# Optimization experiments

Measured on AMD Instinct MI355X. Metric: run time of the kernel, lower is better.

The kernel has to match this reference:

```python
import jax, jax.numpy as jnp
import numpy as np

H = 1024          # hidden_size
M = 512           # moe_intermediate_size
E = 16            # n_routed_experts
TOP_K = 4         # num_experts_per_tok
N_GROUP = 4
TOPK_GROUP = 2
SCALE = 2.5       # routed_scaling_factor
B, S = 2, 1024


def setup_inputs() -> dict:
    key = jax.random.key(0)
    ks = jax.random.split(key, 9)
    sc_h = 1.0 / np.sqrt(H)
    sc_m = 1.0 / np.sqrt(M)
    return {
        "hidden_states": jax.random.normal(ks[0], (B, S, H), jnp.float32),
        "gate_kernel": jax.random.normal(ks[1], (H, E), jnp.float32) * sc_h,
        "gate_bias": jax.random.normal(ks[2], (E,), jnp.float32) * 0.01,
        "w_gate": jax.random.normal(ks[3], (E, H, M), jnp.float32) * sc_h,
        "w_up": jax.random.normal(ks[4], (E, H, M), jnp.float32) * sc_h,
        "w_down": jax.random.normal(ks[5], (E, M, H), jnp.float32) * sc_m,
        "sw_gate": jax.random.normal(ks[6], (H, 2 * M), jnp.float32) * sc_h,
        "sw_up": jax.random.normal(ks[7], (H, 2 * M), jnp.float32) * sc_h,
        "sw_down": jax.random.normal(ks[8], (2 * M, H), jnp.float32) * (1.0 / np.sqrt(2 * M)),
    }


def _gate(x2d, gate_kernel, gate_bias):
    # x2d: [N, H]
    n = x2d.shape[0]
    logits = jnp.dot(x2d.astype(jnp.float32), gate_kernel.astype(jnp.float32))  # [N, E]
    scores = jax.nn.sigmoid(logits)
    scores_for_choice = scores + gate_bias  # noaux_tc correction bias
    # group-limited top-k: sum of top-2 scores per group
    group_scores = scores_for_choice.reshape(n, N_GROUP, E // N_GROUP)
    top2 = jax.lax.top_k(group_scores, k=2)[0]
    group_sum = jnp.sum(top2, axis=-1)                       # [N, G]
    group_idx = jax.lax.top_k(group_sum, k=TOPK_GROUP)[1]    # [N, topk_group]
    group_mask = jnp.zeros_like(group_sum).at[jnp.arange(n)[:, None], group_idx].set(1.0)
    score_mask = jnp.repeat(group_mask[:, :, None], E // N_GROUP, axis=2).reshape(n, E)
    masked_scores = jnp.where(score_mask > 0, scores_for_choice, 0.0)
    topk_weight, topk_idx = jax.lax.top_k(masked_scores, k=TOP_K)
    # norm_topk_prob
    topk_weight = topk_weight / (jnp.sum(topk_weight, axis=-1, keepdims=True) + 1e-20)
    topk_weight = topk_weight * SCALE
    return topk_idx, topk_weight


def reference(hidden_states, gate_kernel, gate_bias, w_gate, w_up, w_down,
              sw_gate, sw_up, sw_down):
    orig_shape = hidden_states.shape
    x = hidden_states.reshape(-1, orig_shape[-1])  # [N, H]
    topk_idx, topk_weight = _gate(x, gate_kernel, gate_bias)
    # combine weight per (token, expert): sum_k (topk_idx==e) * topk_weight
    onehot = (topk_idx[:, :, None] == jnp.arange(E)[None, None, :]).astype(topk_weight.dtype)
    combine = jnp.einsum('nke,nk->ne', onehot, topk_weight)  # [N, E]
    # dense per-expert MLP (faithful to moe_infer which runs every expert)
    g = jnp.einsum('nh,ehm->enm', x, w_gate)   # [E, N, M]
    u = jnp.einsum('nh,ehm->enm', x, w_up)
    inter = jax.nn.silu(g) * u
    y_e = jnp.einsum('enm,emh->enh', inter, w_down)          # [E, N, H]
    y = jnp.einsum('ne,enh->nh', combine, y_e)               # [N, H]
    # shared-expert path
    shared = jnp.dot(jax.nn.silu(jnp.dot(x, sw_gate)) * jnp.dot(x, sw_up), sw_down)
    return (y + shared).reshape(orig_shape)
```

## Files before the change

kernel.cpp:

```cpp
#include <hip/hip_runtime.h>
#include <hip/hip_bf16.h>
#include <cstdint>

#define HID    1024
#define MID    512
#define NEXP   16
#define NTOKS  2048
#define TOPKE  4
#define RSCALE 2.5f
#define CSTR   16

typedef __attribute__((ext_vector_type(8))) short  bf16x8;
typedef __attribute__((ext_vector_type(8))) ushort u16x8;
typedef __attribute__((ext_vector_type(4))) float  f32x4;

__device__ __forceinline__ ushort f2bf(float f){
  unsigned u = __float_as_uint(f);
  u += 0x7fffu + ((u >> 16) & 1u);
  return (ushort)(u >> 16);
}
__device__ __forceinline__ float bf2f(ushort h){ return __uint_as_float(((unsigned)h) << 16); }

#define GLD16(g, l) __builtin_amdgcn_global_load_lds( \
    (const __attribute__((address_space(1))) unsigned int*)(g), \
    (__attribute__((address_space(3))) unsigned int*)(l), 16, 0, 0)

__global__ __launch_bounds__(256) void k_route(const float* __restrict__ x,
                                               const float* __restrict__ gk,
                                               const float* __restrict__ gb,
                                               int* __restrict__ counts,
                                               int* __restrict__ tidx,
                                               float* __restrict__ tw)
{
  __shared__ float sc[16][16];
  __shared__ int lcnt[NEXP];
  const int tid = threadIdx.x;
  const int tl  = tid >> 4;
  const int e   = tid & 15;
  const int t   = blockIdx.x * 16 + tl;

  float acc = 0.f;
  const float* xr = x + (size_t)t * HID;
  for (int h = 0; h < HID; h += 4){
    f32x4 xv = *reinterpret_cast<const f32x4*>(xr + h);
    acc += xv[0] * gk[(h+0)*NEXP + e];
    acc += xv[1] * gk[(h+1)*NEXP + e];
    acc += xv[2] * gk[(h+2)*NEXP + e];
    acc += xv[3] * gk[(h+3)*NEXP + e];
  }
  sc[tl][e] = 1.f / (1.f + expf(-acc)) + gb[e];
  if (tid < NEXP) lcnt[tid] = 0;
  __syncthreads();

  if (tid < 16){
    const int tt = blockIdx.x * 16 + tid;
    float s4[NEXP];
    #pragma unroll
    for (int i = 0; i < NEXP; ++i) s4[i] = sc[tid][i];
    float gs[4];
    #pragma unroll
    for (int g = 0; g < 4; ++g){
      float m1 = -1e30f, m2 = -1e30f;
      #pragma unroll
      for (int j = 0; j < 4; ++j){
        float v = s4[g*4+j];
        if (v > m1){ m2 = m1; m1 = v; } else if (v > m2){ m2 = v; }
      }
      gs[g] = m1 + m2;
    }
    int g1 = 0;
    for (int g = 1; g < 4; ++g) if (gs[g] > gs[g1]) g1 = g;
    int g2 = -1;
    for (int g = 0; g < 4; ++g){
      if (g == g1) continue;
      if (g2 < 0 || gs[g] > gs[g2]) g2 = g;
    }
    float ms[NEXP];
    #pragma unroll
    for (int i = 0; i < NEXP; ++i){
      int g = i >> 2;
      ms[i] = (g == g1 || g == g2) ? s4[i] : 0.0f;
    }
    bool used[NEXP];
    #pragma unroll
    for (int i = 0; i < NEXP; ++i) used[i] = false;
    int sel[TOPKE]; float val[TOPKE]; float denom = 0.f;
    #pragma unroll
    for (int k = 0; k < TOPKE; ++k){
      int be = -1; float bv = -1e30f;
      for (int i = 0; i < NEXP; ++i){
        if (used[i]) continue;
        if (ms[i] > bv){ bv = ms[i]; be = i; }
      }
      used[be] = true; sel[k] = be; val[k] = bv; denom += bv;
    }
    float inv = RSCALE / (denom + 1e-20f);
    #pragma unroll
    for (int k = 0; k < TOPKE; ++k){
      tidx[tt*TOPKE + k] = sel[k];
      tw  [tt*TOPKE + k] = val[k] * inv;
      atomicAdd(&lcnt[sel[k]], 1);
    }
  }
  __syncthreads();
  if (tid < NEXP && lcnt[tid]) atomicAdd(&counts[tid * CSTR], lcnt[tid]);
}

__global__ void k_scan(const int* __restrict__ counts, int* __restrict__ offs,
                       int* __restrict__ cursor)
{
  if (threadIdx.x == 0){
    int s = 0;
    for (int e = 0; e < NEXP; ++e){ offs[e] = s; s += counts[e * CSTR]; }
    offs[NEXP] = s;
  }
  if (threadIdx.x < NEXP) cursor[threadIdx.x * CSTR] = 0;
}

__global__ __launch_bounds__(256) void k_place(const int* __restrict__ tidx,
                                               const float* __restrict__ tw,
                                               const int* __restrict__ offs,
                                               int* __restrict__ cursor,
                                               int* __restrict__ tlist,
                                               float* __restrict__ wlist,
                                               int* __restrict__ pos)
{
  __shared__ int lcnt[NEXP];
  __shared__ int lbase[NEXP];
  const int tid = threadIdx.x;
  const int t = blockIdx.x * 256 + tid;
  if (tid < NEXP) lcnt[tid] = 0;
  __syncthreads();
  int sel[TOPKE]; float w4[TOPKE]; int ls[TOPKE];
  #pragma unroll
  for (int k = 0; k < TOPKE; ++k){
    sel[k] = tidx[t*TOPKE + k];
    w4[k]  = tw[t*TOPKE + k];
    ls[k]  = atomicAdd(&lcnt[sel[k]], 1);
  }
  __syncthreads();
  if (tid < NEXP) lbase[tid] = atomicAdd(&cursor[tid * CSTR], lcnt[tid]);
  __syncthreads();
  #pragma unroll
  for (int k = 0; k < TOPKE; ++k){
    int p = offs[sel[k]] + lbase[sel[k]] + ls[k];
    tlist[p] = t;
    wlist[p] = w4[k];
    pos[t*TOPKE + k] = p;
  }
}

__global__ __launch_bounds__(256) void k_cvt(const float* __restrict__ in,
                                             ushort* __restrict__ out, int n8)
{
  int i = blockIdx.x * 256 + threadIdx.x;
  if (i >= n8) return;
  f32x4 a = *reinterpret_cast<const f32x4*>(in + (size_t)i*8);
  f32x4 b = *reinterpret_cast<const f32x4*>(in + (size_t)i*8 + 4);
  u16x8 o;
  o[0]=f2bf(a[0]); o[1]=f2bf(a[1]); o[2]=f2bf(a[2]); o[3]=f2bf(a[3]);
  o[4]=f2bf(b[0]); o[5]=f2bf(b[1]); o[6]=f2bf(b[2]); o[7]=f2bf(b[3]);
  *reinterpret_cast<u16x8*>(out + (size_t)i*8) = o;
}

__global__ __launch_bounds__(256) void k_tr(const float* __restrict__ in,
                                            ushort* __restrict__ out, int K, int N)
{
  const int e = blockIdx.z;
  in  += (size_t)e * K * N;
  out += (size_t)e * K * N;
  const int kb = blockIdx.y * 64, nb = blockIdx.x * 64;
  __shared__ ushort T[64 * 68];
  const int t = threadIdx.x;
  const int r = t >> 4, c4 = (t & 15) * 4;
  #pragma unroll
  for (int i = 0; i < 4; ++i){
    f32x4 v = *reinterpret_cast<const f32x4*>(in + (size_t)(kb + r + i*16) * N + nb + c4);
    #pragma unroll
    for (int j = 0; j < 4; ++j)
      T[(c4 + j) * 68 + r + i*16] = f2bf(v[j]);
  }
  __syncthreads();
  #pragma unroll
  for (int i = 0; i < 4; ++i){
    int n = r + i*16;
    ushort4 o = *reinterpret_cast<const ushort4*>(&T[n * 68 + c4]);
    *reinterpret_cast<ushort4*>(out + (size_t)(nb + n) * K + kb + c4) = o;
  }
}

__global__ __launch_bounds__(512) void k_mm0(
    const ushort* __restrict__ xb,
    ushort* __restrict__ i_s, ushort* __restrict__ i_r,
    const ushort* __restrict__ swgT, const ushort* __restrict__ swuT,
    const ushort* __restrict__ wgT,  const ushort* __restrict__ wuT,
    const int* __restrict__ counts, const int* __restrict__ offs,
    const int* __restrict__ tlist)
{
  const int z = blockIdx.z;
  const bool routed = (z > 0);
  const int e = z - 1;
  const int N = routed ? 512 : 1024;
  const int nbase = blockIdx.x * 128;
  if (nbase >= N) return;
  const int mbase = blockIdx.y * 128;
  int cnt = NTOKS, aoff = 0;
  if (routed){
    cnt = counts[e * CSTR];
    if (mbase >= cnt) return;
    aoff = offs[e];
  }
  const ushort* Bg = routed ? (wgT + (size_t)e * MID * HID) : swgT;
  const ushort* Bu = routed ? (wuT + (size_t)e * MID * HID) : swuT;
  ushort* O = routed ? i_r : i_s;

  __shared__ __align__(16) ushort Sh[3 * 128 * 64];

  const int tid = threadIdx.x;
  const int l   = tid & 63;
  const int w   = tid >> 6;
  const int wm  = w >> 2;
  const int wn  = w & 3;

  const int rl     = l >> 3;
  const int srcOff = 8 * ((l & 7) ^ rl);

  const ushort* srcP[6];
  #pragma unroll
  for (int j = 0; j < 6; ++j){
    int g = w * 6 + j;
    int b = g >> 4;
    int r = (g & 15) * 8 + rl;
    const ushort* p;
    if (b == 0){
      int ar = mbase + r;
      if (routed){
        int s = aoff + (ar < cnt ? ar : cnt - 1);
        p = xb + (size_t)tlist[s] * HID;
      } else p = xb + (size_t)ar * HID;
    } else if (b == 1){
      p = Bg + (size_t)(nbase + r) * HID;
    } else {
      p = Bu + (size_t)(nbase + r) * HID;
    }
    srcP[j] = p + srcOff;
  }

  f32x4 accg[4][2], accu[4][2];
  #pragma unroll
  for (int i = 0; i < 4; ++i)
    #pragma unroll
    for (int j = 0; j < 2; ++j){
      accg[i][j] = (f32x4){0.f,0.f,0.f,0.f};
      accu[i][j] = (f32x4){0.f,0.f,0.f,0.f};
    }

  const int fr  = l & 15;
  const int ko  = l >> 4;
  const int swz = (fr & 7) << 4;

  for (int kt = 0; kt < 16; ++kt){
    const int ke = kt * 64;
    #pragma unroll
    for (int j = 0; j < 6; ++j)
      GLD16(srcP[j] + ke, (ushort*)Sh + (w*6 + j) * 512);
    __syncthreads();
    #pragma unroll
    for (int ks = 0; ks < 2; ++ks){
      const int co = ks * 64 + ko * 16;
      bf16x8 af[4], bg[2], bu[2];
      #pragma unroll
      for (int mf = 0; mf < 4; ++mf)
        af[mf] = *reinterpret_cast<const bf16x8*>(
            (const char*)Sh + (wm*64 + mf*16 + fr) * 128 + (co ^ swz));
      #pragma unroll
      for (int nf = 0; nf < 2; ++nf){
        int cc = wn*32 + nf*16 + fr;
        bg[nf] = *reinterpret_cast<const bf16x8*>(
            (const char*)Sh + 16384 + cc * 128 + (co ^ swz));
        bu[nf] = *reinterpret_cast<const bf16x8*>(
            (const char*)Sh + 32768 + cc * 128 + (co ^ swz));
      }
      #pragma unroll
      for (int mf = 0; mf < 4; ++mf)
        #pragma unroll
        for (int nf = 0; nf < 2; ++nf){
          accg[mf][nf] = __builtin_amdgcn_mfma_f32_16x16x32_bf16(af[mf], bg[nf], accg[mf][nf], 0, 0, 0);
          accu[mf][nf] = __builtin_amdgcn_mfma_f32_16x16x32_bf16(af[mf], bu[nf], accu[mf][nf], 0, 0, 0);
        }
    }
    __syncthreads();
  }

  const int ccol = l & 15;
  const int crow = (l >> 4) * 4;
  #pragma unroll
  for (int mf = 0; mf < 4; ++mf){
    #pragma unroll
    for (int r_ = 0; r_ < 4; ++r_){
      const int arel = wm*64 + mf*16 + crow + r_ + mbase;
      if (routed && arel >= cnt) continue;
      size_t row = routed ? (size_t)(aoff + arel) : (size_t)arel;
      #pragma unroll
      for (int nf = 0; nf < 2; ++nf){
        int col = nbase + wn*32 + nf*16 + ccol;
        float g = accg[mf][nf][r_];
        float u = accu[mf][nf][r_];
        float s = g / (1.f + expf(-g));
        O[row * N + col] = f2bf(s * u);
      }
    }
  }
}

__global__ __launch_bounds__(512) void k_mm1(
    const ushort* __restrict__ i_s, const ushort* __restrict__ i_r,
    const ushort* __restrict__ swdT, const ushort* __restrict__ wdT,
    ushort* __restrict__ y_s, ushort* __restrict__ y_r,
    const int* __restrict__ counts, const int* __restrict__ offs,
    const float* __restrict__ wlist)
{
  const int z = blockIdx.z;
  const bool routed = (z > 0);
  const int e = z - 1;
  const int Kd = routed ? MID : HID;
  const int mbase = blockIdx.y * 256;
  const int nbase = blockIdx.x * 128;
  int cnt = NTOKS, aoff = 0;
  if (routed){
    cnt = counts[e * CSTR];
    if (mbase >= cnt) return;
    aoff = offs[e];
  }
  const ushort* A = routed ? i_r : i_s;
  const ushort* B = routed ? (wdT + (size_t)e * HID * MID) : swdT;

  __shared__ __align__(16) ushort Sh[3 * 128 * 64];

  const int tid = threadIdx.x;
  const int l   = tid & 63;
  const int w   = tid >> 6;
  const int rg  = w >> 1;
  const int cg  = w & 1;

  const int rl     = l >> 3;
  const int srcOff = 8 * ((l & 7) ^ rl);

  const ushort* srcP[6];
  #pragma unroll
  for (int j = 0; j < 6; ++j){
    int g = w * 6 + j;
    const ushort* p;
    if (g < 32){
      int r = g * 8 + rl;
      int ar = mbase + r;
      if (routed){
        int s = aoff + (ar < cnt ? ar : cnt - 1);
        p = A + (size_t)s * Kd;
      } else p = A + (size_t)ar * Kd;
    } else {
      int r = (g - 32) * 8 + rl;
      p = B + (size_t)(nbase + r) * Kd;
    }
    srcP[j] = p + srcOff;
  }

  f32x4 acc[4][4];
  #pragma unroll
  for (int i = 0; i < 4; ++i)
    #pragma unroll
    for (int j = 0; j < 4; ++j)
      acc[i][j] = (f32x4){0.f,0.f,0.f,0.f};

  const int fr  = l & 15;
  const int ko  = l >> 4;
  const int swz = (fr & 7) << 4;
  const int nk  = Kd >> 6;

  for (int kt = 0; kt < nk; ++kt){
    const int ke = kt * 64;
    #pragma unroll
    for (int j = 0; j < 6; ++j)
      GLD16(srcP[j] + ke, (ushort*)Sh + (w*6 + j) * 512);
    __syncthreads();
    #pragma unroll
    for (int ks = 0; ks < 2; ++ks){
      const int co = ks * 64 + ko * 16;
      bf16x8 af[4], bf[4];
      #pragma unroll
      for (int mf = 0; mf < 4; ++mf)
        af[mf] = *reinterpret_cast<const bf16x8*>(
            (const char*)Sh + (rg*64 + mf*16 + fr) * 128 + (co ^ swz));
      #pragma unroll
      for (int nf = 0; nf < 4; ++nf)
        bf[nf] = *reinterpret_cast<const bf16x8*>(
            (const char*)Sh + 32768 + (cg*64 + nf*16 + fr) * 128 + (co ^ swz));
      #pragma unroll
      for (int mf = 0; mf < 4; ++mf)
        #pragma unroll
        for (int nf = 0; nf < 4; ++nf)
          acc[mf][nf] = __builtin_amdgcn_mfma_f32_16x16x32_bf16(af[mf], bf[nf], acc[mf][nf], 0, 0, 0);
    }
    __syncthreads();
  }

  const int ccol = l & 15;
  const int crow = (l >> 4) * 4;
  #pragma unroll
  for (int mf = 0; mf < 4; ++mf){
    #pragma unroll
    for (int r_ = 0; r_ < 4; ++r_){
      const int arel = rg*64 + mf*16 + crow + r_ + mbase;
      if (routed && arel >= cnt) continue;
      if (!routed){
        #pragma unroll
        for (int nf = 0; nf < 4; ++nf){
          int col = nbase + cg*64 + nf*16 + ccol;
          y_s[(size_t)arel * HID + col] = f2bf(acc[mf][nf][r_]);
        }
      } else {
        int s = aoff + arel;
        float wgt = wlist[s];
        #pragma unroll
        for (int nf = 0; nf < 4; ++nf){
          int col = nbase + cg*64 + nf*16 + ccol;
          y_r[(size_t)s * HID + col] = f2bf(wgt * acc[mf][nf][r_]);
        }
      }
    }
  }
}

__global__ __launch_bounds__(256) void k_comb(const ushort* __restrict__ y_s,
                                              const ushort* __restrict__ y_r,
                                              const int* __restrict__ pos,
                                              float* __restrict__ out)
{
  const int t  = blockIdx.x * 2 + (threadIdx.x >> 7);
  const int c8 = (threadIdx.x & 127) * 8;
  const int* pp = pos + t * TOPKE;
  u16x8 vs = *reinterpret_cast<const u16x8*>(y_s + (size_t)t * HID + c8);
  float s[8];
  #pragma unroll
  for (int j = 0; j < 8; ++j) s[j] = bf2f(vs[j]);
  #pragma unroll
  for (int k = 0; k < TOPKE; ++k){
    int p = pp[k];
    u16x8 vr = *reinterpret_cast<const u16x8*>(y_r + (size_t)p * HID + c8);
    #pragma unroll
    for (int j = 0; j < 8; ++j) s[j] += bf2f(vr[j]);
  }
  f32x4 o0 = (f32x4){s[0],s[1],s[2],s[3]};
  f32x4 o1 = (f32x4){s[4],s[5],s[6],s[7]};
  *reinterpret_cast<f32x4*>(out + (size_t)t * HID + c8)     = o0;
  *reinterpret_cast<f32x4*>(out + (size_t)t * HID + c8 + 4) = o1;
}

extern "C" void kernel_launch(void* const* d_in, const int* in_sizes, int n_in,
                              void* d_out, int out_size, void* d_ws, size_t ws_size,
                              hipStream_t stream)
{
  const float* x   = (const float*)d_in[0];
  const float* gk  = (const float*)d_in[1];
  const float* gb  = (const float*)d_in[2];
  const float* wg  = (const float*)d_in[3];
  const float* wu  = (const float*)d_in[4];
  const float* wd  = (const float*)d_in[5];
  const float* swg = (const float*)d_in[6];
  const float* swu = (const float*)d_in[7];
  const float* swd = (const float*)d_in[8];
  float* out = (float*)d_out;
  char* ws = (char*)d_ws;

  const size_t MB = 1ull << 20;
  int*    counts = (int*)(ws + 0);
  int*    cursor = (int*)(ws + 2048);
  int*    offs   = (int*)(ws + 4096);
  int*    tidx   = (int*)(ws + 8192);
  float*  tw     = (float*)(ws + 49152);
  int*    tlist  = (int*)(ws + 90112);
  float*  wlist  = (float*)(ws + 131072);
  int*    pos    = (int*)(ws + 163840);
  ushort* xb     = (ushort*)(ws + 1*MB);
  ushort* swgT   = (ushort*)(ws + 5*MB);
  ushort* swuT   = (ushort*)(ws + 7*MB);
  ushort* swdT   = (ushort*)(ws + 9*MB);
  ushort* wgT    = (ushort*)(ws + 11*MB);
  ushort* wuT    = (ushort*)(ws + 27*MB);
  ushort* wdT    = (ushort*)(ws + 43*MB);
  ushort* i_s    = (ushort*)(ws + 59*MB);
  ushort* i_r    = (ushort*)(ws + 63*MB);
  ushort* y_r    = (ushort*)(ws + 11*MB);
  ushort* y_s    = (ushort*)(ws + 27*MB);

  hipMemsetAsync(counts, 0, 16 * CSTR * sizeof(int), stream);
  k_route<<<128, 256, 0, stream>>>(x, gk, gb, counts, tidx, tw);
  k_scan<<<1, 64, 0, stream>>>(counts, offs, cursor);
  k_place<<<NTOKS/256, 256, 0, stream>>>(tidx, tw, offs, cursor, tlist, wlist, pos);

  k_cvt<<<1024, 256, 0, stream>>>(x, xb, 262144);
  k_tr<<<dim3(16,16, 1), 256, 0, stream>>>(swg, swgT, 1024, 1024);
  k_tr<<<dim3(16,16, 1), 256, 0, stream>>>(swu, swuT, 1024, 1024);
  k_tr<<<dim3(16,16, 1), 256, 0, stream>>>(swd, swdT, 1024, 1024);
  k_tr<<<dim3( 8,16,16), 256, 0, stream>>>(wg,  wgT,  1024,  512);
  k_tr<<<dim3( 8,16,16), 256, 0, stream>>>(wu,  wuT,  1024,  512);
  k_tr<<<dim3(16, 8,16), 256, 0, stream>>>(wd,  wdT,   512, 1024);

  k_mm0<<<dim3(8,16,17), 512, 0, stream>>>(xb, i_s, i_r, swgT, swuT, wgT, wuT,
                                           counts, offs, tlist);
  k_mm1<<<dim3(8,8,17), 512, 0, stream>>>(i_s, i_r, swdT, wdT, y_s, y_r,
                                          counts, offs, wlist);
  k_comb<<<NTOKS/2, 256, 0, stream>>>(y_s, y_r, pos, out);
}
```

Measured before the change: 182.7 us.

## Double-buffer LDS in expert GEMMs and merge small setup kernels

The two grouped GEMM kernels now keep two LDS buffers, so the global-to-LDS loads for the next K tile are issued while the current tile is being computed, and one barrier per iteration is dropped. The separate scan kernel is removed: expert offsets are recomputed from counts inside the place and GEMM kernels, and the memset now also zeroes the cursor. The six transpose launches are merged into three batched launches to cut launch overhead. Doubling LDS per block (96KB) may lower occupancy.

New measurement: 202.1 us. 1.11x slower.

```diff
diff --git a/kernel.cpp b/kernel.cpp
--- a/kernel.cpp
+++ b/kernel.cpp
@@ -106,20 +106,9 @@
   if (tid < NEXP && lcnt[tid]) atomicAdd(&counts[tid * CSTR], lcnt[tid]);
 }
 
-__global__ void k_scan(const int* __restrict__ counts, int* __restrict__ offs,
-                       int* __restrict__ cursor)
-{
-  if (threadIdx.x == 0){
-    int s = 0;
-    for (int e = 0; e < NEXP; ++e){ offs[e] = s; s += counts[e * CSTR]; }
-    offs[NEXP] = s;
-  }
-  if (threadIdx.x < NEXP) cursor[threadIdx.x * CSTR] = 0;
-}
-
 __global__ __launch_bounds__(256) void k_place(const int* __restrict__ tidx,
                                                const float* __restrict__ tw,
-                                               const int* __restrict__ offs,
+                                               const int* __restrict__ counts,
                                                int* __restrict__ cursor,
                                                int* __restrict__ tlist,
                                                float* __restrict__ wlist,
@@ -127,9 +116,15 @@
 {
   __shared__ int lcnt[NEXP];
   __shared__ int lbase[NEXP];
+  __shared__ int soff[NEXP];
   const int tid = threadIdx.x;
   const int t = blockIdx.x * 256 + tid;
-  if (tid < NEXP) lcnt[tid] = 0;
+  if (tid < NEXP){
+    lcnt[tid] = 0;
+    int s = 0;
+    for (int i = 0; i < tid; ++i) s += counts[i * CSTR];
+    soff[tid] = s;
+  }
   __syncthreads();
   int sel[TOPKE]; float w4[TOPKE]; int ls[TOPKE];
   #pragma unroll
@@ -143,7 +138,7 @@
   __syncthreads();
   #pragma unroll
   for (int k = 0; k < TOPKE; ++k){
-    int p = offs[sel[k]] + lbase[sel[k]] + ls[k];
+    int p = soff[sel[k]] + lbase[sel[k]] + ls[k];
     tlist[p] = t;
     wlist[p] = w4[k];
     pos[t*TOPKE + k] = p;
@@ -163,12 +158,9 @@
   *reinterpret_cast<u16x8*>(out + (size_t)i*8) = o;
 }
 
-__global__ __launch_bounds__(256) void k_tr(const float* __restrict__ in,
-                                            ushort* __restrict__ out, int K, int N)
-{
-  const int e = blockIdx.z;
-  in  += (size_t)e * K * N;
-  out += (size_t)e * K * N;
+__device__ __forceinline__ void tr_body(const float* __restrict__ in,
+                                        ushort* __restrict__ out, int K, int N)
+{
   const int kb = blockIdx.y * 64, nb = blockIdx.x * 64;
   __shared__ ushort T[64 * 68];
   const int t = threadIdx.x;
@@ -187,6 +179,32 @@
     ushort4 o = *reinterpret_cast<const ushort4*>(&T[n * 68 + c4]);
     *reinterpret_cast<ushort4*>(out + (size_t)(nb + n) * K + kb + c4) = o;
   }
+}
+
+__global__ __launch_bounds__(256) void k_trS(const float* __restrict__ a,
+                                             const float* __restrict__ b,
+                                             const float* __restrict__ c,
+                                             ushort* __restrict__ oa,
+                                             ushort* __restrict__ ob,
+                                             ushort* __restrict__ oc)
+{
+  const int z = blockIdx.z;
+  const float* in = (z == 0) ? a : (z == 1) ? b : c;
+  ushort* out     = (z == 0) ? oa : (z == 1) ? ob : oc;
+  tr_body(in, out, 1024, 1024);
+}
+
+__global__ __launch_bounds__(256) void k_trR(const float* __restrict__ a,
+                                             const float* __restrict__ b,
+                                             ushort* __restrict__ oa,
+                                             ushort* __restrict__ ob,
+                                             int K, int N, int split)
+{
+  const int z = blockIdx.z;
+  const int e = z % split;
+  const float* in = ((z < split) ? a : b) + (size_t)e * K * N;
+  ushort* out     = ((z < split) ? oa : ob) + (size_t)e * K * N;
+  tr_body(in, out, K, N);
 }
 
 __global__ __launch_bounds__(512) void k_mm0(
@@ -194,8 +212,7 @@
     ushort* __restrict__ i_s, ushort* __restrict__ i_r,
     const ushort* __restrict__ swgT, const ushort* __restrict__ swuT,
     const ushort* __restrict__ wgT,  const ushort* __restrict__ wuT,
-    const int* __restrict__ counts, const int* __restrict__ offs,
-    const int* __restrict__ tlist)
+    const int* __restrict__ counts, const int* __restrict__ tlist)
 {
   const int z = blockIdx.z;
   const bool routed = (z > 0);
@@ -208,13 +225,13 @@
   if (routed){
     cnt = counts[e * CSTR];
     if (mbase >= cnt) return;
-    aoff = offs[e];
+    for (int i = 0; i < e; ++i) aoff += counts[i * CSTR];
   }
   const ushort* Bg = routed ? (wgT + (size_t)e * MID * HID) : swgT;
   const ushort* Bu = routed ? (wuT + (size_t)e * MID * HID) : swuT;
   ushort* O = routed ? i_r : i_s;
 
-  __shared__ __align__(16) ushort Sh[3 * 128 * 64];
+  __shared__ __align__(16) ushort Sh[2][3 * 128 * 64];
 
   const int tid = threadIdx.x;
   const int l   = tid & 63;
@@ -258,13 +275,22 @@
   const int fr  = l & 15;
   const int ko  = l >> 4;
   const int swz = (fr & 7) << 4;
-
+  const int ldsGrp = (w*6) * 512;
+
+  #pragma unroll
+  for (int j = 0; j < 6; ++j)
+    GLD16(srcP[j], (ushort*)Sh[0] + ldsGrp + j * 512);
+  __syncthreads();
+
+  int cur = 0;
   for (int kt = 0; kt < 16; ++kt){
-    const int ke = kt * 64;
-    #pragma unroll
-    for (int j = 0; j < 6; ++j)
-      GLD16(srcP[j] + ke, (ushort*)Sh + (w*6 + j) * 512);
-    __syncthreads();
+    if (kt + 1 < 16){
+      const int ke = (kt + 1) * 64;
+      #pragma unroll
+      for (int j = 0; j < 6; ++j)
+        GLD16(srcP[j] + ke, (ushort*)Sh[cur ^ 1] + ldsGrp + j * 512);
+    }
+    const char* base = (const char*)Sh[cur];
     #pragma unroll
     for (int ks = 0; ks < 2; ++ks){
       const int co = ks * 64 + ko * 16;
@@ -272,14 +298,12 @@
       #pragma unroll
       for (int mf = 0; mf < 4; ++mf)
         af[mf] = *reinterpret_cast<const bf16x8*>(
-            (const char*)Sh + (wm*64 + mf*16 + fr) * 128 + (co ^ swz));
+            base + (wm*64 + mf*16 + fr) * 128 + (co ^ swz));
       #pragma unroll
       for (int nf = 0; nf < 2; ++nf){
         int cc = wn*32 + nf*16 + fr;
-        bg[nf] = *reinterpret_cast<const bf16x8*>(
-            (const char*)Sh + 16384 + cc * 128 + (co ^ swz));
-        bu[nf] = *reinterpret_cast<const bf16x8*>(
-            (const char*)Sh + 32768 + cc * 128 + (co ^ swz));
+        bg[nf] = *reinterpret_cast<const bf16x8*>(base + 16384 + cc * 128 + (co ^ swz));
+        bu[nf] = *reinterpret_cast<const bf16x8*>(base + 32768 + cc * 128 + (co ^ swz));
       }
       #pragma unroll
       for (int mf = 0; mf < 4; ++mf)
@@ -290,6 +314,7 @@
         }
     }
     __syncthreads();
+    cur ^= 1;
   }
 
   const int ccol = l & 15;
@@ -317,8 +342,7 @@
     const ushort* __restrict__ i_s, const ushort* __restrict__ i_r,
     const ushort* __restrict__ swdT, const ushort* __restrict__ wdT,
     ushort* __restrict__ y_s, ushort* __restrict__ y_r,
-    const int* __restrict__ counts, const int* __restrict__ offs,
-    const float* __restrict__ wlist)
+    const int* __restrict__ counts, const float* __restrict__ wlist)
 {
   const int z = blockIdx.z;
   const bool routed = (z > 0);
@@ -330,12 +354,12 @@
   if (routed){
     cnt = counts[e * CSTR];
     if (mbase >= cnt) return;
-    aoff = offs[e];
+    for (int i = 0; i < e; ++i) aoff += counts[i * CSTR];
   }
   const ushort* A = routed ? i_r : i_s;
   const ushort* B = routed ? (wdT + (size_t)e * HID * MID) : swdT;
 
-  __shared__ __align__(16) ushort Sh[3 * 128 * 64];
+  __shared__ __align__(16) ushort Sh[2][3 * 128 * 64];
 
   const int tid = threadIdx.x;
   const int l   = tid & 63;
@@ -376,13 +400,22 @@
   const int ko  = l >> 4;
   const int swz = (fr & 7) << 4;
   const int nk  = Kd >> 6;
-
+  const int ldsGrp = (w*6) * 512;
+
+  #pragma unroll
+  for (int j = 0; j < 6; ++j)
+    GLD16(srcP[j], (ushort*)Sh[0] + ldsGrp + j * 512);
+  __syncthreads();
+
+  int cur = 0;
   for (int kt = 0; kt < nk; ++kt){
-    const int ke = kt * 64;
-    #pragma unroll
-    for (int j = 0; j < 6; ++j)
-      GLD16(srcP[j] + ke, (ushort*)Sh + (w*6 + j) * 512);
-    __syncthreads();
+    if (kt + 1 < nk){
+      const int ke = (kt + 1) * 64;
+      #pragma unroll
+      for (int j = 0; j < 6; ++j)
+        GLD16(srcP[j] + ke, (ushort*)Sh[cur ^ 1] + ldsGrp + j * 512);
+    }
+    const char* base = (const char*)Sh[cur];
     #pragma unroll
     for (int ks = 0; ks < 2; ++ks){
       const int co = ks * 64 + ko * 16;
@@ -390,11 +423,11 @@
       #pragma unroll
       for (int mf = 0; mf < 4; ++mf)
         af[mf] = *reinterpret_cast<const bf16x8*>(
-            (const char*)Sh + (rg*64 + mf*16 + fr) * 128 + (co ^ swz));
+            base + (rg*64 + mf*16 + fr) * 128 + (co ^ swz));
       #pragma unroll
       for (int nf = 0; nf < 4; ++nf)
         bf[nf] = *reinterpret_cast<const bf16x8*>(
-            (const char*)Sh + 32768 + (cg*64 + nf*16 + fr) * 128 + (co ^ swz));
+            base + 32768 + (cg*64 + nf*16 + fr) * 128 + (co ^ swz));
       #pragma unroll
       for (int mf = 0; mf < 4; ++mf)
         #pragma unroll
@@ -402,6 +435,7 @@
           acc[mf][nf] = __builtin_amdgcn_mfma_f32_16x16x32_bf16(af[mf], bf[nf], acc[mf][nf], 0, 0, 0);
     }
     __syncthreads();
+    cur ^= 1;
   }
 
   const int ccol = l & 15;
@@ -475,7 +509,6 @@
   const size_t MB = 1ull << 20;
   int*    counts = (int*)(ws + 0);
   int*    cursor = (int*)(ws + 2048);
-  int*    offs   = (int*)(ws + 4096);
   int*    tidx   = (int*)(ws + 8192);
   float*  tw     = (float*)(ws + 49152);
   int*    tlist  = (int*)(ws + 90112);
@@ -493,22 +526,18 @@
   ushort* y_r    = (ushort*)(ws + 11*MB);
   ushort* y_s    = (ushort*)(ws + 27*MB);
 
-  hipMemsetAsync(counts, 0, 16 * CSTR * sizeof(int), stream);
+  hipMemsetAsync(ws, 0, 4096, stream);
   k_route<<<128, 256, 0, stream>>>(x, gk, gb, counts, tidx, tw);
-  k_scan<<<1, 64, 0, stream>>>(counts, offs, cursor);
-  k_place<<<NTOKS/256, 256, 0, stream>>>(tidx, tw, offs, cursor, tlist, wlist, pos);
+  k_place<<<NTOKS/256, 256, 0, stream>>>(tidx, tw, counts, cursor, tlist, wlist, pos);
 
   k_cvt<<<1024, 256, 0, stream>>>(x, xb, 262144);
-  k_tr<<<dim3(16,16, 1), 256, 0, stream>>>(swg, swgT, 1024, 1024);
-  k_tr<<<dim3(16,16, 1), 256, 0, stream>>>(swu, swuT, 1024, 1024);
-  k_tr<<<dim3(16,16, 1), 256, 0, stream>>>(swd, swdT, 1024, 1024);
-  k_tr<<<dim3( 8,16,16), 256, 0, stream>>>(wg,  wgT,  1024,  512);
-  k_tr<<<dim3( 8,16,16), 256, 0, stream>>>(wu,  wuT,  1024,  512);
-  k_tr<<<dim3(16, 8,16), 256, 0, stream>>>(wd,  wdT,   512, 1024);
+  k_trS<<<dim3(16,16,3),  256, 0, stream>>>(swg, swu, swd, swgT, swuT, swdT);
+  k_trR<<<dim3( 8,16,32), 256, 0, stream>>>(wg, wu, wgT, wuT, 1024, 512, 16);
+  k_trR<<<dim3(16, 8,16), 256, 0, stream>>>(wd, wd, wdT, wdT, 512, 1024, 16);
 
   k_mm0<<<dim3(8,16,17), 512, 0, stream>>>(xb, i_s, i_r, swgT, swuT, wgT, wuT,
-                                           counts, offs, tlist);
+                                           counts, tlist);
   k_mm1<<<dim3(8,8,17), 512, 0, stream>>>(i_s, i_r, swdT, wdT, y_s, y_r,
-                                          counts, offs, wlist);
+                                          counts, wlist);
   k_comb<<<NTOKS/2, 256, 0, stream>>>(y_s, y_r, pos, out);
 }
```
